# Performance work log

Measured on AMD Instinct MI355X. Metric: run time of the kernel, lower is better.

## Reference

```python
import jax, jax.numpy as jnp
import numpy as np

B, C, H, W = 8, 128, 64, 64   # batch, hidden_dim, spatial
CIN = 192                      # input_dim
N, K, R, DFF = 1, 4, 8, 512    # d_state, scan dirs, dt_rank=ceil(128/16), mlp hidden
EPS = 1e-5


def _conv1x1(t, w, b=None):
    y = jnp.einsum('bchw,oc->bohw', t, w)
    return y + b[None, :, None, None] if b is not None else y


def _ln_cf(t, g, bta):
    # LayerNorm over channel dim (channel_first)
    mu = t.mean(1, keepdims=True)
    var = ((t - mu) ** 2).mean(1, keepdims=True)
    return (t - mu) * jax.lax.rsqrt(var + EPS) * g[None, :, None, None] + bta[None, :, None, None]


def _forward(h, cz, cr, cq, x,
             in_proj_w, in_proj_b, ln1_g, ln1_b,
             ssm_in_w, conv_w, conv_b,
             x_proj_w, dt_w, dt_b, A_logs, Ds,
             outnorm_g, outnorm_b, out_proj_w,
             ln2_g, ln2_b, fc1_w, fc1_b, fc2_w, fc2_b,
             gate_w, gate_b):
    combined = jnp.concatenate([h, x], axis=1)          # [B, C+CIN, H, W]
    feat = _conv1x1(combined, in_proj_w, in_proj_b)     # [B, C, H, W]

    # ---- SS2D (v2_noz, channel_first) ----
    u = _conv1x1(_ln_cf(feat, ln1_g, ln1_b), ssm_in_w)  # in_proj (no bias)
    u = jax.lax.conv_general_dilated(u, conv_w, (1, 1), [(1, 1), (1, 1)],
                                     dimension_numbers=('NCHW', 'OIHW', 'NCHW'),
                                     feature_group_count=C)
    u = jax.nn.silu(u + conv_b[None, :, None, None])

    L = H * W
    x0 = u.reshape(B, C, L)
    x1 = u.transpose(0, 1, 3, 2).reshape(B, C, L)       # column-major scan
    xs = jnp.stack([x0, x1, x0[..., ::-1], x1[..., ::-1]], axis=1)  # [B,K,C,L]

    x_dbl = jnp.einsum('bkcl,kdc->bkdl', xs, x_proj_w)  # [B,K,R+2N,L]
    dts, Bs, Cs = jnp.split(x_dbl, [R, R + N], axis=2)
    delta = jax.nn.softplus(jnp.einsum('bkrl,kcr->bkcl', dts, dt_w) + dt_b[None, :, :, None])
    A = -jnp.exp(A_logs).reshape(K, C, N)
    D = Ds.reshape(K, C)

    dA = jnp.exp(delta[..., None] * A[None, :, :, None, :])                   # [B,K,C,L,N]
    dBu = (delta * xs)[..., None] * Bs.transpose(0, 1, 3, 2)[:, :, None, :, :]  # [B,K,C,L,N]

    def step(hst, inp):
        dA_t, dBu_t, C_t = inp
        hst = dA_t * hst + dBu_t                         # [B,K,C,N]
        return hst, jnp.einsum('bkcn,bkn->bkc', hst, C_t)

    init = jnp.zeros((B, K, C, N), u.dtype)
    _, ys = jax.lax.scan(step, init,
                         (dA.transpose(3, 0, 1, 2, 4),
                          dBu.transpose(3, 0, 1, 2, 4),
                          Cs.transpose(3, 0, 1, 2)))
    ys = ys.transpose(1, 2, 3, 0)                        # [B,K,C,L]
    ys = ys + D[None, :, :, None] * xs

    # cross-merge: undo flips and transposes, sum directions
    y = ys[:, 0] + ys[:, 2, :, ::-1]
    y_t = ys[:, 1] + ys[:, 3, :, ::-1]
    y = y + y_t.reshape(B, C, W, H).transpose(0, 1, 3, 2).reshape(B, C, L)
    y = y.reshape(B, C, H, W)
    y = _ln_cf(y, outnorm_g, outnorm_b)
    ssm_out = _conv1x1(y, out_proj_w)

    # ---- VSSBlock residuals (drop_path identity in eval) ----
    z = feat + ssm_out
    m = _conv1x1(_ln_cf(z, ln2_g, ln2_b), fc1_w, fc1_b)
    m = jax.nn.gelu(m, approximate=False)
    m = _conv1x1(m, fc2_w, fc2_b)
    z = z + m

    # ---- gated update ----
    g = jax.nn.sigmoid(_conv1x1(z, gate_w, gate_b))
    return g * z + (1.0 - g) * h


def setup_inputs() -> dict:
    key = jax.random.key(0)
    ks = jax.random.split(key, 20)
    rn = lambda i, shape, s=0.02: jax.random.normal(ks[i], shape, jnp.float32) * s
    return dict(
        h=jax.random.normal(ks[0], (B, C, H, W), jnp.float32),
        cz=jax.random.normal(ks[1], (B, C, H, W), jnp.float32),
        cr=jax.random.normal(ks[2], (B, C, H, W), jnp.float32),
        cq=jax.random.normal(ks[3], (B, C, H, W), jnp.float32),
        x=jax.random.normal(ks[4], (B, CIN, H, W), jnp.float32),
        in_proj_w=rn(5, (C, C + CIN)), in_proj_b=jnp.zeros(C, jnp.float32),
        ln1_g=jnp.ones(C, jnp.float32), ln1_b=jnp.zeros(C, jnp.float32),
        ssm_in_w=rn(6, (C, C)),
        conv_w=rn(7, (C, 1, 3, 3), 0.1), conv_b=jnp.zeros(C, jnp.float32),
        x_proj_w=rn(8, (K, R + 2 * N, C)),
        dt_w=rn(9, (K, C, R), 0.1), dt_b=rn(10, (K, C), 0.1),
        A_logs=jnp.zeros((K * C, N), jnp.float32),
        Ds=jnp.ones(K * C, jnp.float32),
        outnorm_g=jnp.ones(C, jnp.float32), outnorm_b=jnp.zeros(C, jnp.float32),
        out_proj_w=rn(11, (C, C)),
        ln2_g=jnp.ones(C, jnp.float32), ln2_b=jnp.zeros(C, jnp.float32),
        fc1_w=rn(12, (DFF, C)), fc1_b=jnp.zeros(DFF, jnp.float32),
        fc2_w=rn(13, (C, DFF)), fc2_b=jnp.zeros(C, jnp.float32),
        gate_w=rn(14, (C, C)), gate_b=jnp.zeros(C, jnp.float32),
    )


def reference(h, cz, cr, cq, x,
              in_proj_w, in_proj_b, ln1_g, ln1_b,
              ssm_in_w, conv_w, conv_b,
              x_proj_w, dt_w, dt_b, A_logs, Ds,
              outnorm_g, outnorm_b, out_proj_w,
              ln2_g, ln2_b, fc1_w, fc1_b, fc2_w, fc2_b,
              gate_w, gate_b):
    return _forward(h, cz, cr, cq, x,
                    in_proj_w, in_proj_b, ln1_g, ln1_b,
                    ssm_in_w, conv_w, conv_b,
                    x_proj_w, dt_w, dt_b, A_logs, Ds,
                    outnorm_g, outnorm_b, out_proj_w,
                    ln2_g, ln2_b, fc1_w, fc1_b, fc2_w, fc2_b,
                    gate_w, gate_b)
```

## Files before the change

kernel.cpp:

```cpp
#include <hip/hip_runtime.h>
#include <hip/hip_bf16.h>

constexpr int B_ = 8, C_ = 128, Hh = 64, Ww = 64, L_ = Hh * Ww;
constexpr int CIN_ = 192, K_ = 4, Rr = 8, DFF_ = 512;
constexpr long SZ1 = (long)B_ * C_ * L_;
constexpr float EPSf = 1e-5f;
constexpr float LOG2E = 1.44269504088896f;
constexpr float LN2f  = 0.693147180559945f;

#define DEVI __device__ __forceinline__

using s16x4 = __attribute__((ext_vector_type(4))) short;
using s16x8 = __attribute__((ext_vector_type(8))) short;
using f32x4 = __attribute__((ext_vector_type(4))) float;

DEVI float sigm(float x) { return 1.f / (1.f + __expf(-x)); }
DEVI float geluf(float x) { return 0.5f * x * (1.f + erff(x * 0.70710678118654752f)); }
DEVI float siluf(float x) { return x * sigm(x); }

DEVI unsigned short f2bf(float f) {
    unsigned u = __float_as_uint(f);
    u += 0x7fffu + ((u >> 16) & 1u);
    return (unsigned short)(u >> 16);
}
DEVI float bf2f(unsigned short u) { return __uint_as_float((unsigned)u << 16); }
DEVI float upk(const unsigned* p, int i) {
    unsigned v = p[i >> 1];
    return __uint_as_float((i & 1) ? (v & 0xffff0000u) : (v << 16));
}

DEVI int tadr(int pos) { return ((pos & 63) << 6) | (pos >> 6); }

template <int BN, bool ACC, bool BIAS, bool XGELU, bool SIG, bool GATE, bool SPLIT,
          bool XLN, bool LNOUT, bool XBF, bool OUTBF>
__global__ __launch_bounds__(256) void gemm_k(
    const float* __restrict__ W, const float* __restrict__ X1, long sX1,
    const float* __restrict__ X2, long sX2, int splitRow,
    const float* __restrict__ bias,
    const float* __restrict__ xmu, const float* __restrict__ xrs,
    const float* __restrict__ xg, const float* __restrict__ xbt,
    float* __restrict__ NOut, const float* __restrict__ og, const float* __restrict__ obt,
    float* __restrict__ Cp, long sC, int M, int N, int K)
{
    constexpr int NI = BN / 32;
    __shared__ unsigned short sA[128][40];
    __shared__ unsigned short sB[BN][40];
    const int tid = threadIdx.x;
    const int bn = blockIdx.x, bm = blockIdx.y, bz = blockIdx.z;
    const float* X1b = X1 + (XBF ? 0 : (long)bz * sX1);
    const unsigned short* X1u = XBF ? ((const unsigned short*)X1 + (long)bz * sX1) : nullptr;
    const float* X2b = (SPLIT || GATE) ? (X2 + (long)bz * sX2) : nullptr;
    float* Cb = Cp + (long)bz * sC;
    unsigned short* Cu = OUTBF ? ((unsigned short*)Cp + (long)bz * sC) : nullptr;
    const int n0 = bn * BN, m0 = bm * 128;

    const int l = tid & 63, w = tid >> 6;
    const int wm = w >> 1, wn = w & 1;
    const int lr = l & 15, lk = (l >> 4) * 8;

    const int awrow = tid >> 1, awk = (tid & 1) * 16;

    f32x4 acc[4][NI];
#pragma unroll
    for (int i = 0; i < 4; i++)
#pragma unroll
        for (int j = 0; j < NI; j++) acc[i][j] = (f32x4)0.f;

    for (int k0 = 0; k0 < K; k0 += 32) {
        {
            const float* wp = W + (long)(m0 + awrow) * K + k0 + awk;
            float4 f0 = *(const float4*)(wp + 0);
            float4 f1 = *(const float4*)(wp + 4);
            float4 f2 = *(const float4*)(wp + 8);
            float4 f3 = *(const float4*)(wp + 12);
            s16x8 v0, v1;
            v0[0]=f2bf(f0.x); v0[1]=f2bf(f0.y); v0[2]=f2bf(f0.z); v0[3]=f2bf(f0.w);
            v0[4]=f2bf(f1.x); v0[5]=f2bf(f1.y); v0[6]=f2bf(f1.z); v0[7]=f2bf(f1.w);
            v1[0]=f2bf(f2.x); v1[1]=f2bf(f2.y); v1[2]=f2bf(f2.z); v1[3]=f2bf(f2.w);
            v1[4]=f2bf(f3.x); v1[5]=f2bf(f3.y); v1[6]=f2bf(f3.z); v1[7]=f2bf(f3.w);
            *(s16x8*)&sA[awrow][awk] = v0;
            *(s16x8*)&sA[awrow][awk + 8] = v1;
        }
        if constexpr (BN == 128) {
            const int bnb = tid & 31, bkb = tid >> 5;
            const int krow = k0 + bkb * 4;
            const int colk = n0 + bnb * 4;
            float4 r0, r1, r2, r3;
            if constexpr (XBF) {
                ushort4 a0 = *(const ushort4*)(X1u + (long)krow * N + colk);
                ushort4 a1 = *(const ushort4*)(X1u + (long)(krow + 1) * N + colk);
                ushort4 a2 = *(const ushort4*)(X1u + (long)(krow + 2) * N + colk);
                ushort4 a3 = *(const ushort4*)(X1u + (long)(krow + 3) * N + colk);
                r0 = make_float4(bf2f(a0.x), bf2f(a0.y), bf2f(a0.z), bf2f(a0.w));
                r1 = make_float4(bf2f(a1.x), bf2f(a1.y), bf2f(a1.z), bf2f(a1.w));
                r2 = make_float4(bf2f(a2.x), bf2f(a2.y), bf2f(a2.z), bf2f(a2.w));
                r3 = make_float4(bf2f(a3.x), bf2f(a3.y), bf2f(a3.z), bf2f(a3.w));
            } else {
                const float* xp;
                if (SPLIT && krow >= splitRow)
                    xp = X2b + (long)(krow - splitRow) * N + colk;
                else
                    xp = X1b + (long)krow * N + colk;
                r0 = *(const float4*)(xp + 0 * (long)N);
                r1 = *(const float4*)(xp + 1 * (long)N);
                r2 = *(const float4*)(xp + 2 * (long)N);
                r3 = *(const float4*)(xp + 3 * (long)N);
            }
            if (XGELU) {
                r0.x=geluf(r0.x); r0.y=geluf(r0.y); r0.z=geluf(r0.z); r0.w=geluf(r0.w);
                r1.x=geluf(r1.x); r1.y=geluf(r1.y); r1.z=geluf(r1.z); r1.w=geluf(r1.w);
                r2.x=geluf(r2.x); r2.y=geluf(r2.y); r2.z=geluf(r2.z); r2.w=geluf(r2.w);
                r3.x=geluf(r3.x); r3.y=geluf(r3.y); r3.z=geluf(r3.z); r3.w=geluf(r3.w);
            }
            const float* p0 = (const float*)&r0;
            const float* p1 = (const float*)&r1;
            const float* p2 = (const float*)&r2;
            const float* p3 = (const float*)&r3;
#pragma unroll
            for (int c = 0; c < 4; c++) {
                s16x4 v;
                v[0] = f2bf(p0[c]); v[1] = f2bf(p1[c]);
                v[2] = f2bf(p2[c]); v[3] = f2bf(p3[c]);
                *(s16x4*)&sB[bnb * 4 + c][bkb * 4] = v;
            }
        } else {
            const int bnb = tid & 15, bkb = tid >> 4;
            const int krow = k0 + bkb * 2;
            const int col0 = n0 + bnb * 4;
            float4 r0, r1;
            if constexpr (XBF) {
                ushort4 a0 = *(const ushort4*)(X1u + (long)krow * N + col0);
                ushort4 a1 = *(const ushort4*)(X1u + (long)(krow + 1) * N + col0);
                r0 = make_float4(bf2f(a0.x), bf2f(a0.y), bf2f(a0.z), bf2f(a0.w));
                r1 = make_float4(bf2f(a1.x), bf2f(a1.y), bf2f(a1.z), bf2f(a1.w));
            } else {
                const float* xpa;
                const float* xpb;
                if (SPLIT && krow >= splitRow)
                    xpa = X2b + (long)(krow - splitRow) * N + col0;
                else
                    xpa = X1b + (long)krow * N + col0;
                if (SPLIT && (krow + 1) >= splitRow)
                    xpb = X2b + (long)(krow + 1 - splitRow) * N + col0;
                else
                    xpb = X1b + (long)(krow + 1) * N + col0;
                r0 = *(const float4*)xpa;
                r1 = *(const float4*)xpb;
            }
            if (XLN) {
                float4 m4 = *(const float4*)(xmu + (long)bz * N + col0);
                float4 s4 = *(const float4*)(xrs + (long)bz * N + col0);
                float ga = xg[krow], be = xbt[krow];
                r0.x=(r0.x-m4.x)*s4.x*ga+be; r0.y=(r0.y-m4.y)*s4.y*ga+be;
                r0.z=(r0.z-m4.z)*s4.z*ga+be; r0.w=(r0.w-m4.w)*s4.w*ga+be;
                ga = xg[krow + 1]; be = xbt[krow + 1];
                r1.x=(r1.x-m4.x)*s4.x*ga+be; r1.y=(r1.y-m4.y)*s4.y*ga+be;
                r1.z=(r1.z-m4.z)*s4.z*ga+be; r1.w=(r1.w-m4.w)*s4.w*ga+be;
            }
            if (XGELU) {
                r0.x=geluf(r0.x); r0.y=geluf(r0.y); r0.z=geluf(r0.z); r0.w=geluf(r0.w);
                r1.x=geluf(r1.x); r1.y=geluf(r1.y); r1.z=geluf(r1.z); r1.w=geluf(r1.w);
            }
            const float* p0 = (const float*)&r0;
            const float* p1 = (const float*)&r1;
#pragma unroll
            for (int c = 0; c < 4; c++) {
                unsigned v = (unsigned)f2bf(p0[c]) | ((unsigned)f2bf(p1[c]) << 16);
                *(unsigned*)&sB[bnb * 4 + c][bkb * 2] = v;
            }
        }
        __syncthreads();
        s16x8 af[4], bf[NI];
#pragma unroll
        for (int mi = 0; mi < 4; mi++) af[mi] = *(const s16x8*)&sA[wm * 64 + mi * 16 + lr][lk];
#pragma unroll
        for (int ni = 0; ni < NI; ni++) bf[ni] = *(const s16x8*)&sB[wn * (BN / 2) + ni * 16 + lr][lk];
#pragma unroll
        for (int mi = 0; mi < 4; mi++)
#pragma unroll
            for (int ni = 0; ni < NI; ni++)
                acc[mi][ni] = __builtin_amdgcn_mfma_f32_16x16x32_bf16(af[mi], bf[ni], acc[mi][ni], 0, 0, 0);
        __syncthreads();
    }

    float ps[NI], pq[NI];
    if (LNOUT) {
#pragma unroll
        for (int ni = 0; ni < NI; ni++) { ps[ni] = 0.f; pq[ni] = 0.f; }
    }
#pragma unroll
    for (int mi = 0; mi < 4; mi++) {
#pragma unroll
        for (int r = 0; r < 4; r++) {
            const int row = m0 + wm * 64 + mi * 16 + (l >> 4) * 4 + r;
            const float bv = BIAS ? bias[row] : 0.f;
#pragma unroll
            for (int ni = 0; ni < NI; ni++) {
                const int col = n0 + wn * (BN / 2) + ni * 16 + lr;
                float v = acc[mi][ni][r] + bv;
                if constexpr (OUTBF) {
                    Cu[(long)row * N + col] = f2bf(v);
                } else {
                    float* cp = Cb + (long)row * N + col;
                    if (ACC) v += *cp;
                    if (SIG) v = sigm(v);
                    if (GATE) {
                        v = sigm(v);
                        float zv = X1b[(long)row * N + col];
                        float hv = X2b[(long)row * N + col];
                        v = hv + v * (zv - hv);
                    }
                    *cp = v;
                }
                if (LNOUT) {
                    acc[mi][ni][r] = v;
                    ps[ni] += v; pq[ni] += v * v;
                }
            }
        }
    }
    if constexpr (LNOUT) {
        __shared__ float redS[2][2][NI][16];
        __shared__ float redQ[2][2][NI][16];
        __shared__ float muL[BN], rsL[BN];
#pragma unroll
        for (int ni = 0; ni < NI; ni++) {
            ps[ni] += __shfl_xor(ps[ni], 16, 64);
            ps[ni] += __shfl_xor(ps[ni], 32, 64);
            pq[ni] += __shfl_xor(pq[ni], 16, 64);
            pq[ni] += __shfl_xor(pq[ni], 32, 64);
        }
        if (l < 16) {
#pragma unroll
            for (int ni = 0; ni < NI; ni++) {
                redS[wm][wn][ni][l] = ps[ni];
                redQ[wm][wn][ni][l] = pq[ni];
            }
        }
        __syncthreads();
        if (tid < BN) {
            const int cc = tid;
            const int wn2 = cc >> 5, rem = cc & 31;
            const int ni2 = rem >> 4, lr2 = rem & 15;
            float s = redS[0][wn2][ni2][lr2] + redS[1][wn2][ni2][lr2];
            float q = redQ[0][wn2][ni2][lr2] + redQ[1][wn2][ni2][lr2];
            float mu = s * (1.f / 128.f);
            float var = q * (1.f / 128.f) - mu * mu;
            muL[cc] = mu;
            rsL[cc] = rsqrtf(var + EPSf);
        }
        __syncthreads();
        unsigned short* Nb = (unsigned short*)NOut + (long)bz * sC;
#pragma unroll
        for (int mi = 0; mi < 4; mi++) {
#pragma unroll
            for (int r = 0; r < 4; r++) {
                const int row = m0 + wm * 64 + mi * 16 + (l >> 4) * 4 + r;
                const float gg = og[row], bb = obt[row];
#pragma unroll
                for (int ni = 0; ni < NI; ni++) {
                    const int cc = wn * (BN / 2) + ni * 16 + lr;
                    const int col = n0 + cc;
                    float v = acc[mi][ni][r];
                    Nb[(long)row * N + col] = f2bf((v - muL[cc]) * rsL[cc] * gg + bb);
                }
            }
        }
    }
}

__global__ __launch_bounds__(256) void ln_stats_k(const unsigned short* __restrict__ in,
                                                  float* __restrict__ mu,
                                                  float* __restrict__ rs)
{
    __shared__ float s1[4][64], s2[4][64];
    const int tid = threadIdx.x;
    const int p = tid & 63, q = tid >> 6;
    const long posg = (long)blockIdx.x * 64 + p;
    const int b = (int)(posg / L_);
    const int pp = (int)(posg % L_);
    const unsigned short* base = in + ((long)b * C_ + q * 32) * L_ + pp;
    float s = 0.f, sq = 0.f;
#pragma unroll
    for (int i = 0; i < 32; i++) {
        float t = bf2f(base[(long)i * L_]);
        s += t; sq += t * t;
    }
    s1[q][p] = s; s2[q][p] = sq;
    __syncthreads();
    if (q == 0) {
        float ts = s1[0][p] + s1[1][p] + s1[2][p] + s1[3][p];
        float tq = s2[0][p] + s2[1][p] + s2[2][p] + s2[3][p];
        float m = ts * (1.f / 128.f);
        float var = tq * (1.f / 128.f) - m * m;
        mu[posg] = m;
        rs[posg] = rsqrtf(var + EPSf);
    }
}

__global__ __launch_bounds__(256) void dwconvT_k(const unsigned short* __restrict__ in,
                                                 const float* __restrict__ wts,
                                                 const float* __restrict__ bias,
                                                 unsigned short* __restrict__ uo,
                                                 unsigned short* __restrict__ uTo)
{
    __shared__ float t[64][65];
    const long plane = blockIdx.x;
    const int c = (int)(plane & 127);
    const int tid = threadIdx.x;
    const unsigned short* src = in + plane * (long)L_;
#pragma unroll
    for (int ii = 0; ii < 16; ii++) {
        int idx = tid + ii * 256;
        t[idx >> 6][idx & 63] = bf2f(src[idx]);
    }
    float kw[9];
#pragma unroll
    for (int q = 0; q < 9; q++) kw[q] = wts[c * 9 + q];
    const float bc = bias[c];
    __syncthreads();
    float r[16];
#pragma unroll
    for (int ii = 0; ii < 16; ii++) {
        int idx = tid + ii * 256;
        int h = idx >> 6, w2 = idx & 63;
        float acc = bc;
#pragma unroll
        for (int dh = -1; dh <= 1; dh++) {
            int hh = h + dh;
            if ((unsigned)hh >= 64u) continue;
#pragma unroll
            for (int dw = -1; dw <= 1; dw++) {
                int ww2 = w2 + dw;
                if ((unsigned)ww2 >= 64u) continue;
                acc += t[hh][ww2] * kw[(dh + 1) * 3 + (dw + 1)];
            }
        }
        r[ii] = siluf(acc);
    }
    __syncthreads();
    unsigned short* ud = uo + plane * (long)L_;
#pragma unroll
    for (int ii = 0; ii < 16; ii++) {
        int idx = tid + ii * 256;
        t[idx >> 6][idx & 63] = r[ii];
        ud[idx] = f2bf(r[ii]);
    }
    __syncthreads();
    unsigned short* utd = uTo + plane * (long)L_;
#pragma unroll
    for (int ii = 0; ii < 16; ii++) {
        int idx = tid + ii * 256;
        utd[idx] = f2bf(t[idx & 63][idx >> 6]);
    }
}

__global__ __launch_bounds__(256) void transpb_k(const unsigned short* __restrict__ src,
                                                 unsigned short* __restrict__ dst)
{
    __shared__ float t[64][65];
    const long plane = blockIdx.x;
    const unsigned short* s = src + plane * (long)L_;
    unsigned short* d = dst + plane * (long)L_;
    const int tid = threadIdx.x;
#pragma unroll
    for (int i = 0; i < 16; i++) {
        int idx = tid + i * 256;
        t[idx >> 6][idx & 63] = bf2f(s[idx]);
    }
    __syncthreads();
#pragma unroll
    for (int i = 0; i < 16; i++) {
        int idx = tid + i * 256;
        int r = idx >> 6, cc = idx & 63;
        float val = t[cc][r] + bf2f(d[idx]);
        d[idx] = f2bf(val);
    }
}

__global__ __launch_bounds__(256) void xdbl2_k(const unsigned short* __restrict__ u,
                                               const unsigned short* __restrict__ uT,
                                               const float* __restrict__ xw,
                                               float* __restrict__ out)
{
    __shared__ float wsm[2][16][132];
    const int pair = blockIdx.y, b = blockIdx.z;
    const int tid = threadIdx.x;
#pragma unroll
    for (int i = 0; i < 8; i++) {
        int idx = tid * 8 + i;
        wsm[0][idx >> 7][idx & 127] = xw[pair * 2048 + idx];
        wsm[1][idx >> 7][idx & 127] = xw[(pair + 2) * 2048 + idx];
    }
    __syncthreads();
    const int dg = (tid & 3) * 4;
    const int lo = tid >> 2;
    const int pos = blockIdx.x * 64 + lo;
    const unsigned short* usrc = (pair ? uT : u) + (long)b * C_ * L_ + pos;
    float a0[4] = {0.f, 0.f, 0.f, 0.f};
    float a1[4] = {0.f, 0.f, 0.f, 0.f};
#pragma unroll 4
    for (int c = 0; c < C_; c++) {
        float uc = bf2f(usrc[(long)c * L_]);
#pragma unroll
        for (int j = 0; j < 4; j++) {
            a0[j] += wsm[0][dg + j][c] * uc;
            a1[j] += wsm[1][dg + j][c] * uc;
        }
    }
    const long baseA = ((long)(b * K_ + pair) * L_) << 4;
    const long baseB = ((long)(b * K_ + pair + 2) * L_) << 4;
    const int s  = tadr(pos);
    const int s2 = tadr(L_ - 1 - pos);
    *(float4*)(out + baseA + ((long)s  << 4) + dg) = make_float4(a0[0], a0[1], a0[2], a0[3]);
    *(float4*)(out + baseB + ((long)s2 << 4) + dg) = make_float4(a1[0], a1[1], a1[2], a1[3]);
}

template <bool WV>
__global__ __launch_bounds__(256) void scan_ph1L_k(const float* __restrict__ xdbl,
                                                   const unsigned short* __restrict__ u,
                                                   const unsigned short* __restrict__ uT,
                                                   const float* __restrict__ dtw,
                                                   const float* __restrict__ dtb,
                                                   const float* __restrict__ alogs,
                                                   float* __restrict__ st,
                                                   unsigned short* __restrict__ wvb)
{
    __shared__ float xtf[2][32][16];
    __shared__ float xtb[2][32][16];
    const int bid = blockIdx.x;
    const int jj = bid & 63, kh = (bid >> 6) & 1, b = bid >> 7;
    const int t = threadIdx.x;
    const int kf = kh, kb = kh + 2;
    const float* xf = xdbl + ((long)(b * 4 + kf) << 16);
    const float* xb = xdbl + ((long)(b * 4 + kb) << 16);
    {
        const int q = t & 3, i = (t >> 2) & 31, j2 = t >> 7;
        const int jf = 2 * jj + j2, jB = 127 - jf;
        const int sf = (((jf & 1) * 32 + i) << 6) | (jf >> 1);
        const int sb = (((jB & 1) * 32 + i) << 6) | (jB >> 1);
        *(float4*)&xtf[j2][i][q * 4] = *(const float4*)(xf + (long)sf * 16 + q * 4);
        *(float4*)&xtb[j2][i][q * 4] = *(const float4*)(xb + (long)sb * 16 + q * 4);
    }
    const int c = t & 127, jh = t >> 7;
    const int jf = 2 * jj + jh, jB = 127 - jf;
    const unsigned short* uplane = (kh ? uT : u) + (long)(b * 128 + c) * L_;
    unsigned ur2[16];
    {
        const unsigned short* up = uplane + jf * 32;
#pragma unroll
        for (int q = 0; q < 4; q++) {
            uint4 a = *(const uint4*)(up + q * 8);
            ur2[q * 4 + 0] = a.x; ur2[q * 4 + 1] = a.y;
            ur2[q * 4 + 2] = a.z; ur2[q * 4 + 3] = a.w;
        }
    }
    __syncthreads();
    unsigned wv2[16];
    {
        float dw[8];
#pragma unroll
        for (int r = 0; r < 8; r++) dw[r] = dtw[((kf * 128 + c) << 3) + r];
        const float db = dtb[kf * 128 + c];
        float An[4];
#pragma unroll
        for (int n = 0; n < 4; n++) An[n] = -__expf(alogs[((kf * 128 + c) << 2) + n]);
        float P0 = 1.f, P1 = 1.f, P2 = 1.f, P3 = 1.f;
        float S0 = 0.f, S1 = 0.f, S2 = 0.f, S3 = 0.f;
#pragma unroll
        for (int i = 0; i < 32; i++) {
            float4 x0 = *(const float4*)&xtf[jh][i][0];
            float4 x1 = *(const float4*)&xtf[jh][i][4];
            float4 xs = *(const float4*)&xtf[jh][i][8];
            float z = db + x0.x*dw[0] + x0.y*dw[1] + x0.z*dw[2] + x0.w*dw[3]
                         + x1.x*dw[4] + x1.y*dw[5] + x1.z*dw[6] + x1.w*dw[7];
            float wv = (z > 15.f) ? z * LOG2E : log2f(1.f + __expf(z));
            unsigned short wb = f2bf(wv);
            wv = bf2f(wb);
            if (i & 1) wv2[i >> 1] |= ((unsigned)wb << 16);
            else       wv2[i >> 1]  = (unsigned)wb;
            float dl = wv * LN2f;
            float du = dl * upk(ur2, i);
            float e;
            e = exp2f(wv * An[0]); S0 = e * S0 + du * xs.x; P0 *= e;
            e = exp2f(wv * An[1]); S1 = e * S1 + du * xs.y; P1 *= e;
            e = exp2f(wv * An[2]); S2 = e * S2 + du * xs.z; P2 *= e;
            e = exp2f(wv * An[3]); S3 = e * S3 + du * xs.w; P3 *= e;
        }
        float* o = st + ((long)((b * 4 + kf) * 128 + c) << 10) + (jf << 3);
        *(float4*)o = make_float4(P0, P1, P2, P3);
        *(float4*)(o + 4) = make_float4(S0, S1, S2, S3);
        if constexpr (WV) {
            unsigned short* wd = wvb + ((long)((b * 4 + kf) * 128 + c) << 12) + jf * 32;
#pragma unroll
            for (int q = 0; q < 4; q++)
                *(uint4*)(wd + q * 8) = make_uint4(wv2[q*4], wv2[q*4+1], wv2[q*4+2], wv2[q*4+3]);
        }
    }
    {
        float dw[8];
#pragma unroll
        for (int r = 0; r < 8; r++) dw[r] = dtw[((kb * 128 + c) << 3) + r];
        const float db = dtb[kb * 128 + c];
        float An[4];
#pragma unroll
        for (int n = 0; n < 4; n++) An[n] = -__expf(alogs[((kb * 128 + c) << 2) + n]);
        float P0 = 1.f, P1 = 1.f, P2 = 1.f, P3 = 1.f;
        float S0 = 0.f, S1 = 0.f, S2 = 0.f, S3 = 0.f;
#pragma unroll
        for (int i = 0; i < 32; i++) {
            float4 x0 = *(const float4*)&xtb[jh][i][0];
            float4 x1 = *(const float4*)&xtb[jh][i][4];
            float4 xs = *(const float4*)&xtb[jh][i][8];
            float z = db + x0.x*dw[0] + x0.y*dw[1] + x0.z*dw[2] + x0.w*dw[3]
                         + x1.x*dw[4] + x1.y*dw[5] + x1.z*dw[6] + x1.w*dw[7];
            float wv = (z > 15.f) ? z * LOG2E : log2f(1.f + __expf(z));
            unsigned short wb = f2bf(wv);
            wv = bf2f(wb);
            if (i & 1) wv2[i >> 1] |= ((unsigned)wb << 16);
            else       wv2[i >> 1]  = (unsigned)wb;
            float dl = wv * LN2f;
            float du = dl * upk(ur2, 31 - i);
            float e;
            e = exp2f(wv * An[0]); S0 = e * S0 + du * xs.x; P0 *= e;
            e = exp2f(wv * An[1]); S1 = e * S1 + du * xs.y; P1 *= e;
            e = exp2f(wv * An[2]); S2 = e * S2 + du * xs.z; P2 *= e;
            e = exp2f(wv * An[3]); S3 = e * S3 + du * xs.w; P3 *= e;
        }
        float* o = st + ((long)((b * 4 + kb) * 128 + c) << 10) + (jB << 3);
        *(float4*)o = make_float4(P0, P1, P2, P3);
        *(float4*)(o + 4) = make_float4(S0, S1, S2, S3);
        if constexpr (WV) {
            unsigned short* wd = wvb + ((long)((b * 4 + kb) * 128 + c) << 12) + jB * 32;
#pragma unroll
            for (int q = 0; q < 4; q++)
                *(uint4*)(wd + q * 8) = make_uint4(wv2[q*4], wv2[q*4+1], wv2[q*4+2], wv2[q*4+3]);
        }
    }
}

__global__ __launch_bounds__(256) void scan_mid_k(float* __restrict__ st)
{
    const long t = (long)blockIdx.x * 256 + threadIdx.x;
    const long chain = t >> 6;
    const int ln = (int)(t & 63);
    float* base = st + (chain << 10) + (ln << 4);
    float4 Pa = *(float4*)(base + 0);
    float4 Sa = *(float4*)(base + 4);
    float4 Pb = *(float4*)(base + 8);
    float4 Sb = *(float4*)(base + 12);
    float4 P, S;
    P.x = Pb.x * Pa.x; P.y = Pb.y * Pa.y; P.z = Pb.z * Pa.z; P.w = Pb.w * Pa.w;
    S.x = Sb.x + Pb.x * Sa.x; S.y = Sb.y + Pb.y * Sa.y;
    S.z = Sb.z + Pb.z * Sa.z; S.w = Sb.w + Pb.w * Sa.w;
#pragma unroll
    for (int d = 1; d < 64; d <<= 1) {
        float4 Pu, Su;
        Pu.x = __shfl_up(P.x, d, 64); Pu.y = __shfl_up(P.y, d, 64);
        Pu.z = __shfl_up(P.z, d, 64); Pu.w = __shfl_up(P.w, d, 64);
        Su.x = __shfl_up(S.x, d, 64); Su.y = __shfl_up(S.y, d, 64);
        Su.z = __shfl_up(S.z, d, 64); Su.w = __shfl_up(S.w, d, 64);
        if (ln >= d) {
            S.x += P.x * Su.x; S.y += P.y * Su.y;
            S.z += P.z * Su.z; S.w += P.w * Su.w;
            P.x *= Pu.x; P.y *= Pu.y; P.z *= Pu.z; P.w *= Pu.w;
        }
    }
    float4 E;
    E.x = __shfl_up(S.x, 1, 64); E.y = __shfl_up(S.y, 1, 64);
    E.z = __shfl_up(S.z, 1, 64); E.w = __shfl_up(S.w, 1, 64);
    if (ln == 0) { E.x = 0.f; E.y = 0.f; E.z = 0.f; E.w = 0.f; }
    float4 E1;
    E1.x = Sa.x + Pa.x * E.x; E1.y = Sa.y + Pa.y * E.y;
    E1.z = Sa.z + Pa.z * E.z; E1.w = Sa.w + Pa.w * E.w;
    *(float4*)(base + 4)  = E;
    *(float4*)(base + 12) = E1;
}

template <bool WV>
__global__ __launch_bounds__(256) void scan_ph2L_k(const float* __restrict__ xdbl,
                                                   const unsigned short* __restrict__ u,
                                                   const unsigned short* __restrict__ uT,
                                                   const float* __restrict__ dtw,
                                                   const float* __restrict__ dtb,
                                                   const float* __restrict__ alogs,
                                                   const float* __restrict__ Dsp,
                                                   const float* __restrict__ st,
                                                   const unsigned short* __restrict__ wvb,
                                                   unsigned short* __restrict__ Y0,
                                                   unsigned short* __restrict__ Yt)
{
    constexpr int TS = WV ? 8 : 16;
    __shared__ float xtf[2][32][TS];
    __shared__ float xtb[2][32][TS];
    const int bid = blockIdx.x;
    const int jj = bid & 63, kh = (bid >> 6) & 1, b = bid >> 7;
    const int t = threadIdx.x;
    const int kf = kh, kb = kh + 2;
    const float* xf = xdbl + ((long)(b * 4 + kf) << 16);
    const float* xb = xdbl + ((long)(b * 4 + kb) << 16);
    if constexpr (WV) {
        const int tt = t & 127;
        const int q = tt & 1, i = (tt >> 1) & 31, j2 = tt >> 6;
        const int jf2 = 2 * jj + j2, jB2 = 127 - jf2;
        if (t < 128) {
            const int sf = (((jf2 & 1) * 32 + i) << 6) | (jf2 >> 1);
            *(float4*)&xtf[j2][i][q * 4] = *(const float4*)(xf + (long)sf * 16 + 8 + q * 4);
        } else {
            const int sb = (((jB2 & 1) * 32 + i) << 6) | (jB2 >> 1);
            *(float4*)&xtb[j2][i][q * 4] = *(const float4*)(xb + (long)sb * 16 + 8 + q * 4);
        }
    } else {
        const int q = t & 3, i = (t >> 2) & 31, j2 = t >> 7;
        const int jf2 = 2 * jj + j2, jB2 = 127 - jf2;
        const int sf = (((jf2 & 1) * 32 + i) << 6) | (jf2 >> 1);
        const int sb = (((jB2 & 1) * 32 + i) << 6) | (jB2 >> 1);
        *(float4*)&xtf[j2][i][q * 4] = *(const float4*)(xf + (long)sf * 16 + q * 4);
        *(float4*)&xtb[j2][i][q * 4] = *(const float4*)(xb + (long)sb * 16 + q * 4);
    }
    const int c = t & 127, jh = t >> 7;
    const int jf = 2 * jj + jh, jB = 127 - jf;
    const unsigned short* uplane = (kh ? uT : u) + (long)(b * 128 + c) * L_;
    unsigned ur2[16];
    {
        const unsigned short* up = uplane + jf * 32;
#pragma unroll
        for (int q = 0; q < 4; q++) {
            uint4 a = *(const uint4*)(up + q * 8);
            ur2[q * 4 + 0] = a.x; ur2[q * 4 + 1] = a.y;
            ur2[q * 4 + 2] = a.z; ur2[q * 4 + 3] = a.w;
        }
    }
    __syncthreads();
    float yreg[32];
    unsigned wv2[16];
    {
        float An[4];
#pragma unroll
        for (int n = 0; n < 4; n++) An[n] = -__expf(alogs[((kf * 128 + c) << 2) + n]);
        const float Dc = Dsp[kf * 128 + c];
        float dw[8]; float db = 0.f;
        if constexpr (!WV) {
#pragma unroll
            for (int r = 0; r < 8; r++) dw[r] = dtw[((kf * 128 + c) << 3) + r];
            db = dtb[kf * 128 + c];
        } else {
            const unsigned short* wp2 = wvb + ((long)((b * 4 + kf) * 128 + c) << 12) + jf * 32;
#pragma unroll
            for (int q = 0; q < 4; q++) {
                uint4 a = *(const uint4*)(wp2 + q * 8);
                wv2[q * 4 + 0] = a.x; wv2[q * 4 + 1] = a.y;
                wv2[q * 4 + 2] = a.z; wv2[q * 4 + 3] = a.w;
            }
        }
        float4 H = *(const float4*)(st + ((long)((b * 4 + kf) * 128 + c) << 10) + (jf << 3) + 4);
        float h0 = H.x, h1 = H.y, h2 = H.z, h3 = H.w;
#pragma unroll
        for (int i = 0; i < 32; i++) {
            float wv;
            if constexpr (WV) {
                wv = upk(wv2, i);
            } else {
                float4 x0 = *(const float4*)&xtf[jh][i][0];
                float4 x1 = *(const float4*)&xtf[jh][i][4];
                float z = db + x0.x*dw[0] + x0.y*dw[1] + x0.z*dw[2] + x0.w*dw[3]
                             + x1.x*dw[4] + x1.y*dw[5] + x1.z*dw[6] + x1.w*dw[7];
                wv = (z > 15.f) ? z * LOG2E : log2f(1.f + __expf(z));
            }
            float4 xs = *(const float4*)&xtf[jh][i][TS - 8];
            float4 xc = *(const float4*)&xtf[jh][i][TS - 4];
            float uv = upk(ur2, i);
            float dl = wv * LN2f;
            float du = dl * uv;
            float e;
            e = exp2f(wv * An[0]); h0 = e * h0 + du * xs.x;
            e = exp2f(wv * An[1]); h1 = e * h1 + du * xs.y;
            e = exp2f(wv * An[2]); h2 = e * h2 + du * xs.z;
            e = exp2f(wv * An[3]); h3 = e * h3 + du * xs.w;
            yreg[i] = h0 * xc.x + h1 * xc.y + h2 * xc.z + h3 * xc.w + Dc * uv;
        }
    }
    {
        float An[4];
#pragma unroll
        for (int n = 0; n < 4; n++) An[n] = -__expf(alogs[((kb * 128 + c) << 2) + n]);
        const float Dc = Dsp[kb * 128 + c];
        float dw[8]; float db = 0.f;
        if constexpr (!WV) {
#pragma unroll
            for (int r = 0; r < 8; r++) dw[r] = dtw[((kb * 128 + c) << 3) + r];
            db = dtb[kb * 128 + c];
        } else {
            const unsigned short* wp2 = wvb + ((long)((b * 4 + kb) * 128 + c) << 12) + jB * 32;
#pragma unroll
            for (int q = 0; q < 4; q++) {
                uint4 a = *(const uint4*)(wp2 + q * 8);
                wv2[q * 4 + 0] = a.x; wv2[q * 4 + 1] = a.y;
                wv2[q * 4 + 2] = a.z; wv2[q * 4 + 3] = a.w;
            }
        }
        float4 H = *(const float4*)(st + ((long)((b * 4 + kb) * 128 + c) << 10) + (jB << 3) + 4);
        float h0 = H.x, h1 = H.y, h2 = H.z, h3 = H.w;
#pragma unroll
        for (int i = 0; i < 32; i++) {
            float wv;
            if constexpr (WV) {
                wv = upk(wv2, i);
            } else {
                float4 x0 = *(const float4*)&xtb[jh][i][0];
                float4 x1 = *(const float4*)&xtb[jh][i][4];
                float z = db + x0.x*dw[0] + x0.y*dw[1] + x0.z*dw[2] + x0.w*dw[3]
                             + x1.x*dw[4] + x1.y*dw[5] + x1.z*dw[6] + x1.w*dw[7];
                wv = (z > 15.f) ? z * LOG2E : log2f(1.f + __expf(z));
            }
            float4 xs = *(const float4*)&xtb[jh][i][TS - 8];
            float4 xc = *(const float4*)&xtb[jh][i][TS - 4];
            float uv = upk(ur2, 31 - i);
            float dl = wv * LN2f;
            float du = dl * uv;
            float e;
            e = exp2f(wv * An[0]); h0 = e * h0 + du * xs.x;
            e = exp2f(wv * An[1]); h1 = e * h1 + du * xs.y;
            e = exp2f(wv * An[2]); h2 = e * h2 + du * xs.z;
            e = exp2f(wv * An[3]); h3 = e * h3 + du * xs.w;
            yreg[31 - i] += h0 * xc.x + h1 * xc.y + h2 * xc.z + h3 * xc.w + Dc * uv;
        }
    }
    unsigned short* ydst = (kh ? Yt : Y0) + (long)(b * 128 + c) * L_ + jf * 32;
#pragma unroll
    for (int q = 0; q < 8; q++) {
        ushort4 v;
        v.x = f2bf(yreg[q * 4 + 0]); v.y = f2bf(yreg[q * 4 + 1]);
        v.z = f2bf(yreg[q * 4 + 2]); v.w = f2bf(yreg[q * 4 + 3]);
        *(ushort4*)(ydst + q * 4) = v;
    }
}

extern "C" void kernel_launch(void* const* d_in, const int* in_sizes, int n_in,
                              void* d_out, int out_size, void* d_ws, size_t ws_size,
                              hipStream_t stream)
{
    const float* h_in      = (const float*)d_in[0];
    const float* x_in      = (const float*)d_in[4];
    const float* in_proj_w = (const float*)d_in[5];
    const float* in_proj_b = (const float*)d_in[6];
    const float* ln1_g     = (const float*)d_in[7];
    const float* ln1_b     = (const float*)d_in[8];
    const float* ssm_in_w  = (const float*)d_in[9];
    const float* conv_w    = (const float*)d_in[10];
    const float* conv_b    = (const float*)d_in[11];
    const float* x_proj_w  = (const float*)d_in[12];
    const float* dt_w      = (const float*)d_in[13];
    const float* dt_b      = (const float*)d_in[14];
    const float* A_logs    = (const float*)d_in[15];
    const float* Dsp       = (const float*)d_in[16];
    const float* outnorm_g = (const float*)d_in[17];
    const float* outnorm_b = (const float*)d_in[18];
    const float* out_proj_w= (const float*)d_in[19];
    const float* ln2_g     = (const float*)d_in[20];
    const float* ln2_b     = (const float*)d_in[21];
    const float* fc1_w     = (const float*)d_in[22];
    const float* fc1_b     = (const float*)d_in[23];
    const float* fc2_w     = (const float*)d_in[24];
    const float* fc2_b     = (const float*)d_in[25];
    const float* gate_w    = (const float*)d_in[26];
    const float* gate_b    = (const float*)d_in[27];

    float* ws   = (float*)d_ws;
    float* fz   = ws;
    float* ubuf = ws + SZ1;
    float* tbuf = ws + 2 * SZ1;
    float* ybuf = ws + 3 * SZ1;
    float* xdbl = ws + 4 * SZ1;
    float* stbf = ws + 4 * SZ1 + 2097152;
    float* muB  = stbf;
    float* rsB  = stbf + 32768;
    const long wvOff = 4 * SZ1 + 2097152 + 4194304;
    unsigned short* wvb = (unsigned short*)(ws + wvOff);
    const bool wvOK = (ws_size / 4) >= (size_t)(wvOff + 8388608);
    float* mbuf = ubuf;
    float* gbuf = (float*)d_out;

    unsigned short* u_u  = (unsigned short*)ubuf;
    unsigned short* u0_u = (unsigned short*)tbuf;
    unsigned short* uT_u = (unsigned short*)ybuf;
    unsigned short* y0_u = (unsigned short*)tbuf;
    unsigned short* yt_u = (unsigned short*)gbuf;

    const dim3 blk(256);
    const long sBC = (long)C_ * L_;
    const long sX  = (long)CIN_ * L_;
    const long sM  = (long)DFF_ * L_;

    gemm_k<64, false, true, false, false, false, true, false, true, false, false>
        <<<dim3(64, 1, 8), blk, 0, stream>>>(
        in_proj_w, h_in, sBC, x_in, sX, 128, in_proj_b,
        nullptr, nullptr, nullptr, nullptr, ybuf, ln1_g, ln1_b,
        fz, sBC, 128, L_, 320);
    gemm_k<64, false, false, false, false, false, false, false, false, true, true>
        <<<dim3(64, 1, 8), blk, 0, stream>>>(
        ssm_in_w, ybuf, sBC, nullptr, 0, 1 << 30, nullptr,
        nullptr, nullptr, nullptr, nullptr, nullptr, nullptr, nullptr,
        tbuf, sBC, 128, L_, 128);
    dwconvT_k<<<dim3(1024), blk, 0, stream>>>(u0_u, conv_w, conv_b, u_u, uT_u);
    xdbl2_k<<<dim3(64, 2, 8), blk, 0, stream>>>(u_u, uT_u, x_proj_w, xdbl);
    if (wvOK) {
        scan_ph1L_k<true><<<dim3(1024), blk, 0, stream>>>(xdbl, u_u, uT_u, dt_w, dt_b,
                                                          A_logs, stbf, wvb);
        scan_mid_k<<<dim3(1024), blk, 0, stream>>>(stbf);
        scan_ph2L_k<true><<<dim3(1024), blk, 0, stream>>>(xdbl, u_u, uT_u, dt_w, dt_b,
                                                          A_logs, Dsp, stbf, wvb, y0_u, yt_u);
    } else {
        scan_ph1L_k<false><<<dim3(1024), blk, 0, stream>>>(xdbl, u_u, uT_u, dt_w, dt_b,
                                                           A_logs, stbf, wvb);
        scan_mid_k<<<dim3(1024), blk, 0, stream>>>(stbf);
        scan_ph2L_k<false><<<dim3(1024), blk, 0, stream>>>(xdbl, u_u, uT_u, dt_w, dt_b,
                                                           A_logs, Dsp, stbf, wvb, y0_u, yt_u);
    }
    transpb_k<<<dim3(1024), blk, 0, stream>>>(yt_u, y0_u);
    ln_stats_k<<<dim3(512), blk, 0, stream>>>(y0_u, muB, rsB);
    gemm_k<64, true, false, false, false, false, false, true, true, true, false>
        <<<dim3(64, 1, 8), blk, 0, stream>>>(
        out_proj_w, tbuf, sBC, nullptr, 0, 1 << 30, nullptr,
        muB, rsB, outnorm_g, outnorm_b, gbuf, ln2_g, ln2_b,
        fz, sBC, 128, L_, 128);
    gemm_k<128, false, true, false, false, false, false, false, false, true, true>
        <<<dim3(32, 4, 8), blk, 0, stream>>>(
        fc1_w, gbuf, sBC, nullptr, 0, 1 << 30, fc1_b,
        nullptr, nullptr, nullptr, nullptr, nullptr, nullptr, nullptr,
        mbuf, sM, 512, L_, 128);
    gemm_k<64, true, true, true, false, false, false, false, false, true, false>
        <<<dim3(64, 1, 8), blk, 0, stream>>>(
        fc2_w, mbuf, sM, nullptr, 0, 1 << 30, fc2_b,
        nullptr, nullptr, nullptr, nullptr, nullptr, nullptr, nullptr,
        fz, sBC, 128, L_, 512);
    gemm_k<64, false, true, false, false, true, false, false, false, false, false>
        <<<dim3(64, 1, 8), blk, 0, stream>>>(
        gate_w, fz, sBC, h_in, sBC, 1 << 30, gate_b,
        nullptr, nullptr, nullptr, nullptr, nullptr, nullptr, nullptr,
        (float*)d_out, sBC, 128, L_, 128);
}
```

Measured before the change: 226.7 us.

## Fuse ssm_in and gate GEMMs into preceding GEMM epilogues; simplify scan products

The LN1 output tile is staged in shared memory and multiplied by ssm_in_w inside the in_proj GEMM. The fc2 output is likewise staged and fed to the gate GEMM, whose sigmoid blend with h is written straight to the output. Two launches and their intermediate global round-trips go away. In scan phase 1 the running products of exp terms are replaced by a single exp of the summed delta, and the unused fourth float4 of x_dbl is no longer loaded. The cost is much larger static shared memory per block (about 50KB), which may lower occupancy.

```diff
diff --git a/kernel.cpp b/kernel.cpp
--- a/kernel.cpp
+++ b/kernel.cpp
@@ -32,7 +32,7 @@
 DEVI int tadr(int pos) { return ((pos & 63) << 6) | (pos >> 6); }
 
 template <int BN, bool ACC, bool BIAS, bool XGELU, bool SIG, bool GATE, bool SPLIT,
-          bool XLN, bool LNOUT, bool XBF, bool OUTBF>
+          bool XLN, bool LNOUT, bool XBF, bool OUTBF, int F2>
 __global__ __launch_bounds__(256) void gemm_k(
     const float* __restrict__ W, const float* __restrict__ X1, long sX1,
     const float* __restrict__ X2, long sX2, int splitRow,
@@ -40,11 +40,15 @@
     const float* __restrict__ xmu, const float* __restrict__ xrs,
     const float* __restrict__ xg, const float* __restrict__ xbt,
     float* __restrict__ NOut, const float* __restrict__ og, const float* __restrict__ obt,
-    float* __restrict__ Cp, long sC, int M, int N, int K)
+    float* __restrict__ Cp, long sC, int M, int N, int K,
+    const float* __restrict__ W2, const float* __restrict__ b2,
+    const float* __restrict__ Hres, float* __restrict__ Out2)
 {
     constexpr int NI = BN / 32;
     __shared__ unsigned short sA[128][40];
     __shared__ unsigned short sB[BN][40];
+    constexpr int F2S = (F2 > 0) ? (128 * 136 + 64 * 136) : 1;
+    __shared__ unsigned short s2buf[F2S];
     const int tid = threadIdx.x;
     const int bn = blockIdx.x, bm = blockIdx.y, bz = blockIdx.z;
     const float* X1b = X1 + (XBF ? 0 : (long)bz * sX1);
@@ -170,16 +174,16 @@
             }
         }
         __syncthreads();
-        s16x8 af[4], bf[NI];
+        s16x8 af[4], bfr[NI];
 #pragma unroll
         for (int mi = 0; mi < 4; mi++) af[mi] = *(const s16x8*)&sA[wm * 64 + mi * 16 + lr][lk];
 #pragma unroll
-        for (int ni = 0; ni < NI; ni++) bf[ni] = *(const s16x8*)&sB[wn * (BN / 2) + ni * 16 + lr][lk];
+        for (int ni = 0; ni < NI; ni++) bfr[ni] = *(const s16x8*)&sB[wn * (BN / 2) + ni * 16 + lr][lk];
 #pragma unroll
         for (int mi = 0; mi < 4; mi++)
 #pragma unroll
             for (int ni = 0; ni < NI; ni++)
-                acc[mi][ni] = __builtin_amdgcn_mfma_f32_16x16x32_bf16(af[mi], bf[ni], acc[mi][ni], 0, 0, 0);
+                acc[mi][ni] = __builtin_amdgcn_mfma_f32_16x16x32_bf16(af[mi], bfr[ni], acc[mi][ni], 0, 0, 0);
         __syncthreads();
     }
 
@@ -196,7 +200,8 @@
             const float bv = BIAS ? bias[row] : 0.f;
 #pragma unroll
             for (int ni = 0; ni < NI; ni++) {
-                const int col = n0 + wn * (BN / 2) + ni * 16 + lr;
+                const int colL = wn * (BN / 2) + ni * 16 + lr;
+                const int col = n0 + colL;
                 float v = acc[mi][ni][r] + bv;
                 if constexpr (OUTBF) {
                     Cu[(long)row * N + col] = f2bf(v);
@@ -210,7 +215,12 @@
                         float hv = X2b[(long)row * N + col];
                         v = hv + v * (zv - hv);
                     }
-                    *cp = v;
+                    if constexpr (F2 == 2) {
+                        s2buf[128 * 136 + colL * 136 + row] = f2bf(v);
+                        acc[mi][ni][r] = v;
+                    } else {
+                        *cp = v;
+                    }
                 }
                 if (LNOUT) {
                     acc[mi][ni][r] = v;
@@ -262,7 +272,70 @@
                     const int cc = wn * (BN / 2) + ni * 16 + lr;
                     const int col = n0 + cc;
                     float v = acc[mi][ni][r];
-                    Nb[(long)row * N + col] = f2bf((v - muL[cc]) * rsL[cc] * gg + bb);
+                    float nv = (v - muL[cc]) * rsL[cc] * gg + bb;
+                    if constexpr (F2 == 1)
+                        s2buf[128 * 136 + cc * 136 + row] = f2bf(nv);
+                    else
+                        Nb[(long)row * N + col] = f2bf(nv);
+                }
+            }
+        }
+    }
+    if constexpr (F2 > 0) {
+        {
+            const int r2 = tid >> 1, kk = (tid & 1) * 16;
+#pragma unroll
+            for (int q = 0; q < 4; q++) {
+                const float* wp = W2 + (long)r2 * 128 + q * 32 + kk;
+                float4 f0 = *(const float4*)(wp + 0);
+                float4 f1 = *(const float4*)(wp + 4);
+                float4 f2 = *(const float4*)(wp + 8);
+                float4 f3 = *(const float4*)(wp + 12);
+                s16x8 v0, v1;
+                v0[0]=f2bf(f0.x); v0[1]=f2bf(f0.y); v0[2]=f2bf(f0.z); v0[3]=f2bf(f0.w);
+                v0[4]=f2bf(f1.x); v0[5]=f2bf(f1.y); v0[6]=f2bf(f1.z); v0[7]=f2bf(f1.w);
+                v1[0]=f2bf(f2.x); v1[1]=f2bf(f2.y); v1[2]=f2bf(f2.z); v1[3]=f2bf(f2.w);
+                v1[4]=f2bf(f3.x); v1[5]=f2bf(f3.y); v1[6]=f2bf(f3.z); v1[7]=f2bf(f3.w);
+                *(s16x8*)&s2buf[r2 * 136 + q * 32 + kk] = v0;
+                *(s16x8*)&s2buf[r2 * 136 + q * 32 + kk + 8] = v1;
+            }
+        }
+        __syncthreads();
+        f32x4 acc2[4][2];
+#pragma unroll
+        for (int i = 0; i < 4; i++) { acc2[i][0] = (f32x4)0.f; acc2[i][1] = (f32x4)0.f; }
+#pragma unroll
+        for (int k0 = 0; k0 < 4; k0++) {
+            s16x8 af2[4], bf2[2];
+#pragma unroll
+            for (int mi = 0; mi < 4; mi++)
+                af2[mi] = *(const s16x8*)&s2buf[(wm * 64 + mi * 16 + lr) * 136 + k0 * 32 + lk];
+#pragma unroll
+            for (int ni = 0; ni < 2; ni++)
+                bf2[ni] = *(const s16x8*)&s2buf[128 * 136 + (wn * 32 + ni * 16 + lr) * 136 + k0 * 32 + lk];
+#pragma unroll
+            for (int mi = 0; mi < 4; mi++)
+#pragma unroll
+                for (int ni = 0; ni < 2; ni++)
+                    acc2[mi][ni] = __builtin_amdgcn_mfma_f32_16x16x32_bf16(af2[mi], bf2[ni], acc2[mi][ni], 0, 0, 0);
+        }
+#pragma unroll
+        for (int mi = 0; mi < 4; mi++) {
+#pragma unroll
+            for (int r = 0; r < 4; r++) {
+                const int row = wm * 64 + mi * 16 + (l >> 4) * 4 + r;
+#pragma unroll
+                for (int ni = 0; ni < 2; ni++) {
+                    const int col = n0 + wn * 32 + ni * 16 + lr;
+                    float v2 = acc2[mi][ni][r];
+                    if constexpr (F2 == 1) {
+                        ((unsigned short*)Out2 + (long)bz * sC)[(long)row * N + col] = f2bf(v2);
+                    } else {
+                        float g = sigm(v2 + b2[row]);
+                        float zv = acc[mi][ni][r];
+                        float hv = Hres[(long)bz * sC + (long)row * N + col];
+                        (Out2 + (long)bz * sC)[(long)row * N + col] = hv + g * (zv - hv);
+                    }
                 }
             }
         }
@@ -426,8 +499,8 @@
                                                    float* __restrict__ st,
                                                    unsigned short* __restrict__ wvb)
 {
-    __shared__ float xtf[2][32][16];
-    __shared__ float xtb[2][32][16];
+    __shared__ float xtf[2][32][12];
+    __shared__ float xtb[2][32][12];
     const int bid = blockIdx.x;
     const int jj = bid & 63, kh = (bid >> 6) & 1, b = bid >> 7;
     const int t = threadIdx.x;
@@ -436,11 +509,13 @@
     const float* xb = xdbl + ((long)(b * 4 + kb) << 16);
     {
         const int q = t & 3, i = (t >> 2) & 31, j2 = t >> 7;
-        const int jf = 2 * jj + j2, jB = 127 - jf;
-        const int sf = (((jf & 1) * 32 + i) << 6) | (jf >> 1);
-        const int sb = (((jB & 1) * 32 + i) << 6) | (jB >> 1);
-        *(float4*)&xtf[j2][i][q * 4] = *(const float4*)(xf + (long)sf * 16 + q * 4);
-        *(float4*)&xtb[j2][i][q * 4] = *(const float4*)(xb + (long)sb * 16 + q * 4);
+        if (q < 3) {
+            const int jf = 2 * jj + j2, jB = 127 - jf;
+            const int sf = (((jf & 1) * 32 + i) << 6) | (jf >> 1);
+            const int sb = (((jB & 1) * 32 + i) << 6) | (jB >> 1);
+            *(float4*)&xtf[j2][i][q * 4] = *(const float4*)(xf + (long)sf * 16 + q * 4);
+            *(float4*)&xtb[j2][i][q * 4] = *(const float4*)(xb + (long)sb * 16 + q * 4);
+        }
     }
     const int c = t & 127, jh = t >> 7;
     const int jf = 2 * jj + jh, jB = 127 - jf;
@@ -465,7 +540,7 @@
         float An[4];
 #pragma unroll
         for (int n = 0; n < 4; n++) An[n] = -__expf(alogs[((kf * 128 + c) << 2) + n]);
-        float P0 = 1.f, P1 = 1.f, P2 = 1.f, P3 = 1.f;
+        float wsum = 0.f;
         float S0 = 0.f, S1 = 0.f, S2 = 0.f, S3 = 0.f;
 #pragma unroll
         for (int i = 0; i < 32; i++) {
@@ -479,16 +554,18 @@
             wv = bf2f(wb);
             if (i & 1) wv2[i >> 1] |= ((unsigned)wb << 16);
             else       wv2[i >> 1]  = (unsigned)wb;
+            wsum += wv;
             float dl = wv * LN2f;
             float du = dl * upk(ur2, i);
             float e;
-            e = exp2f(wv * An[0]); S0 = e * S0 + du * xs.x; P0 *= e;
-            e = exp2f(wv * An[1]); S1 = e * S1 + du * xs.y; P1 *= e;
-            e = exp2f(wv * An[2]); S2 = e * S2 + du * xs.z; P2 *= e;
-            e = exp2f(wv * An[3]); S3 = e * S3 + du * xs.w; P3 *= e;
+            e = exp2f(wv * An[0]); S0 = e * S0 + du * xs.x;
+            e = exp2f(wv * An[1]); S1 = e * S1 + du * xs.y;
+            e = exp2f(wv * An[2]); S2 = e * S2 + du * xs.z;
+            e = exp2f(wv * An[3]); S3 = e * S3 + du * xs.w;
         }
         float* o = st + ((long)((b * 4 + kf) * 128 + c) << 10) + (jf << 3);
-        *(float4*)o = make_float4(P0, P1, P2, P3);
+        *(float4*)o = make_float4(exp2f(wsum * An[0]), exp2f(wsum * An[1]),
+                                  exp2f(wsum * An[2]), exp2f(wsum * An[3]));
         *(float4*)(o + 4) = make_float4(S0, S1, S2, S3);
         if constexpr (WV) {
             unsigned short* wd = wvb + ((long)((b * 4 + kf) * 128 + c) << 12) + jf * 32;
@@ -505,7 +582,7 @@
         float An[4];
 #pragma unroll
         for (int n = 0; n < 4; n++) An[n] = -__expf(alogs[((kb * 128 + c) << 2) + n]);
-        float P0 = 1.f, P1 = 1.f, P2 = 1.f, P3 = 1.f;
+        float wsum = 0.f;
         float S0 = 0.f, S1 = 0.f, S2 = 0.f, S3 = 0.f;
 #pragma unroll
         for (int i = 0; i < 32; i++) {
@@ -519,16 +596,18 @@
             wv = bf2f(wb);
             if (i & 1) wv2[i >> 1] |= ((unsigned)wb << 16);
             else       wv2[i >> 1]  = (unsigned)wb;
+            wsum += wv;
             float dl = wv * LN2f;
             float du = dl * upk(ur2, 31 - i);
             float e;
-            e = exp2f(wv * An[0]); S0 = e * S0 + du * xs.x; P0 *= e;
-            e = exp2f(wv * An[1]); S1 = e * S1 + du * xs.y; P1 *= e;
-            e = exp2f(wv * An[2]); S2 = e * S2 + du * xs.z; P2 *= e;
-            e = exp2f(wv * An[3]); S3 = e * S3 + du * xs.w; P3 *= e;
+            e = exp2f(wv * An[0]); S0 = e * S0 + du * xs.x;
+            e = exp2f(wv * An[1]); S1 = e * S1 + du * xs.y;
+            e = exp2f(wv * An[2]); S2 = e * S2 + du * xs.z;
+            e = exp2f(wv * An[3]); S3 = e * S3 + du * xs.w;
         }
         float* o = st + ((long)((b * 4 + kb) * 128 + c) << 10) + (jB << 3);
-        *(float4*)o = make_float4(P0, P1, P2, P3);
+        *(float4*)o = make_float4(exp2f(wsum * An[0]), exp2f(wsum * An[1]),
+                                  exp2f(wsum * An[2]), exp2f(wsum * An[3]));
         *(float4*)(o + 4) = make_float4(S0, S1, S2, S3);
         if constexpr (WV) {
             unsigned short* wd = wvb + ((long)((b * 4 + kb) * 128 + c) << 12) + jB * 32;
@@ -792,16 +871,12 @@
     const long sX  = (long)CIN_ * L_;
     const long sM  = (long)DFF_ * L_;
 
-    gemm_k<64, false, true, false, false, false, true, false, true, false, false>
+    gemm_k<64, false, true, false, false, false, true, false, true, false, false, 1>
         <<<dim3(64, 1, 8), blk, 0, stream>>>(
         in_proj_w, h_in, sBC, x_in, sX, 128, in_proj_b,
-        nullptr, nullptr, nullptr, nullptr, ybuf, ln1_g, ln1_b,
-        fz, sBC, 128, L_, 320);
-    gemm_k<64, false, false, false, false, false, false, false, false, true, true>
-        <<<dim3(64, 1, 8), blk, 0, stream>>>(
-        ssm_in_w, ybuf, sBC, nullptr, 0, 1 << 30, nullptr,
-        nullptr, nullptr, nullptr, nullptr, nullptr, nullptr, nullptr,
-        tbuf, sBC, 128, L_, 128);
+        nullptr, nullptr, nullptr, nullptr, nullptr, ln1_g, ln1_b,
+        fz, sBC, 128, L_, 320,
+        ssm_in_w, nullptr, nullptr, tbuf);
     dwconvT_k<<<dim3(1024), blk, 0, stream>>>(u0_u, conv_w, conv_b, u_u, uT_u);
     xdbl2_k<<<dim3(64, 2, 8), blk, 0, stream>>>(u_u, uT_u, x_proj_w, xdbl);
     if (wvOK) {
@@ -819,24 +894,22 @@
     }
     transpb_k<<<dim3(1024), blk, 0, stream>>>(yt_u, y0_u);
     ln_stats_k<<<dim3(512), blk, 0, stream>>>(y0_u, muB, rsB);
-    gemm_k<64, true, false, false, false, false, false, true, true, true, false>
+    gemm_k<64, true, false, false, false, false, false, true, true, true, false, 0>
         <<<dim3(64, 1, 8), blk, 0, stream>>>(
         out_proj_w, tbuf, sBC, nullptr, 0, 1 << 30, nullptr,
         muB, rsB, outnorm_g, outnorm_b, gbuf, ln2_g, ln2_b,
-        fz, sBC, 128, L_, 128);
-    gemm_k<128, false, true, false, false, false, false, false, false, true, true>
+        fz, sBC, 128, L_, 128,
+        nullptr, nullptr, nullptr, nullptr);
+    gemm_k<128, false, true, false, false, false, false, false, false, true, true, 0>
         <<<dim3(32, 4, 8), blk, 0, stream>>>(
         fc1_w, gbuf, sBC, nullptr, 0, 1 << 30, fc1_b,
         nullptr, nullptr, nullptr, nullptr, nullptr, nullptr, nullptr,
-        mbuf, sM, 512, L_, 128);
-    gemm_k<64, true, true, true, false, false, false, false, false, true, false>
+        mbuf, sM, 512, L_, 128,
+        nullptr, nullptr, nullptr, nullptr);
+    gemm_k<64, true, true, true, false, false, false, false, false, true, false, 2>
         <<<dim3(64, 1, 8), blk, 0, stream>>>(
         fc2_w, mbuf, sM, nullptr, 0, 1 << 30, fc2_b,
         nullptr, nullptr, nullptr, nullptr, nullptr, nullptr, nullptr,
-        fz, sBC, 128, L_, 512);
-    gemm_k<64, false, true, false, false, true, false, false, false, false, false>
-        <<<dim3(64, 1, 8), blk, 0, stream>>>(
-        gate_w, fz, sBC, h_in, sBC, 1 << 30, gate_b,
-        nullptr, nullptr, nullptr, nullptr, nullptr, nullptr, nullptr,
-        (float*)d_out, sBC, 128, L_, 128);
-}
+        fz, sBC, 128, L_, 512,
+        gate_w, gate_b, h_in, (float*)d_out);
+}
```

Measured after the change: 210.8 us (median of 4 runs). -7.0%, faster.
